# Kernel tuning notes

Hardware: AMD Instinct MI355X
Metric: run time of the kernel (lower is better)

## Reference

```python
import jax, jax.numpy as jnp
import numpy as np

N, M, D = 8192, 8192, 512

def setup_inputs() -> dict:
    key = jax.random.key(0)
    kx, ky = jax.random.split(key)
    x = jax.random.normal(kx, (N, D), dtype=jnp.float32)
    y = jax.random.normal(ky, (M, D), dtype=jnp.float32)
    gamma = jnp.ones((1,), dtype=jnp.float32)
    return {"x": x, "y": y, "gamma": gamma}

def reference(x, y, gamma):
    # Flatten leading dims as in the torch module
    x = x.reshape(-1, x.shape[-1])  # (N, D)
    y = y.reshape(-1, y.shape[-1])  # (M, D)
    x2 = jnp.sum(x * x, axis=-1)  # (N,)
    y2 = jnp.sum(y * y, axis=-1)  # (M,)
    xy = jnp.einsum('nd,md->nm', x, y)  # (N, M)
    sq_norm = x2[:, None] + y2[None, :] - 2.0 * xy
    return jnp.exp(-gamma[0] * sq_norm)
```

## Files before the change

kernel.cpp:

```cpp
#include <hip/hip_runtime.h>

#define NROWS 8192
#define DDIM  512
#define OUTN  8192

typedef int   i32x4  __attribute__((ext_vector_type(4)));
typedef int   i32x8  __attribute__((ext_vector_type(8)));
typedef float f32x16 __attribute__((ext_vector_type(16)));

__global__ void __launch_bounds__(256)
rbf_prep(const float* __restrict__ x, const float* __restrict__ y,
         unsigned char* __restrict__ xs, unsigned char* __restrict__ ys,
         float* __restrict__ x2, float* __restrict__ y2) {
    __shared__ unsigned char lbuf[16384];
    const int tid  = threadIdx.x;
    const int lane = tid & 63;
    const int w    = tid >> 6;

    int grp = blockIdx.x;
    const float* src; unsigned char* dst; float* nrm;
    if (grp < 256) { src = x; dst = xs; nrm = x2; }
    else           { grp -= 256; src = y; dst = ys; nrm = y2; }

    const int loff_base = (lane >> 3) * 2048 + ((lane >> 2) & 1) * 1024 + (lane & 3) * 8;

#pragma unroll
    for (int j = 0; j < 8; ++j) {
        const int r   = w * 8 + j;
        const int row = grp * 32 + r;
        const float* p = src + (size_t)row * DDIM + lane * 8;
        float4 v0 = *(const float4*)(p);
        float4 v1 = *(const float4*)(p + 4);

        float s = v0.x * v0.x + v0.y * v0.y + v0.z * v0.z + v0.w * v0.w
                + v1.x * v1.x + v1.y * v1.y + v1.z * v1.z + v1.w * v1.w;

        int lo = __builtin_amdgcn_cvt_pk_fp8_f32(v0.x, v0.y, 0, false);
        lo     = __builtin_amdgcn_cvt_pk_fp8_f32(v0.z, v0.w, lo, true);
        int hi = __builtin_amdgcn_cvt_pk_fp8_f32(v1.x, v1.y, 0, false);
        hi     = __builtin_amdgcn_cvt_pk_fp8_f32(v1.z, v1.w, hi, true);

        *(int2*)(lbuf + loff_base + r * 32) = make_int2(lo, hi);

#pragma unroll
        for (int o = 32; o > 0; o >>= 1) s += __shfl_down(s, o, 64);
        if (lane == 0) nrm[row] = s;
    }

    __syncthreads();
    unsigned char* gdst = dst + (size_t)grp * 16384;
#pragma unroll
    for (int it = 0; it < 4; ++it)
        *(i32x4*)(gdst + it * 4096 + tid * 16) =
            *(const i32x4*)(lbuf + it * 4096 + tid * 16);
}

__global__ void __launch_bounds__(256, 3)
rbf_gemm(const unsigned char* __restrict__ xs,
         const unsigned char* __restrict__ ys,
         const float* __restrict__ x2, const float* __restrict__ y2,
         const float* __restrict__ gamma, float* __restrict__ out) {
    const int tid  = threadIdx.x;
    const int lane = tid & 63;
    const int w    = tid >> 6;
    const int wm   = w & 1;
    const int wn   = w >> 1;

    const int bm = blockIdx.x & 63;
    const int bn = blockIdx.x >> 6;
    const int row0 = bm * 128;
    const int col0 = bn * 128;

    f32x16 acc[2][2] = {};

    const unsigned char* abase = xs + (size_t)(bm * 4 + wm * 2) * 16384 + lane * 32;
    const unsigned char* bbase = ys + (size_t)(bn * 4 + wn * 2) * 16384 + lane * 32;

#pragma unroll 2
    for (int h = 0; h < 8; ++h) {
        i32x8 af[2], bf[2];
#pragma unroll
        for (int mi = 0; mi < 2; ++mi) {
            const unsigned char* p = abase + mi * 16384 + h * 2048;
            i32x4 lo = *(const i32x4*)(p);
            i32x4 hi = *(const i32x4*)(p + 16);
            af[mi] = __builtin_shufflevector(lo, hi, 0, 1, 2, 3, 4, 5, 6, 7);
        }
#pragma unroll
        for (int ni = 0; ni < 2; ++ni) {
            const unsigned char* p = bbase + ni * 16384 + h * 2048;
            i32x4 lo = *(const i32x4*)(p);
            i32x4 hi = *(const i32x4*)(p + 16);
            bf[ni] = __builtin_shufflevector(lo, hi, 0, 1, 2, 3, 4, 5, 6, 7);
        }
#pragma unroll
        for (int mi = 0; mi < 2; ++mi)
#pragma unroll
            for (int ni = 0; ni < 2; ++ni)
                acc[mi][ni] = __builtin_amdgcn_mfma_scale_f32_32x32x64_f8f6f4(
                    af[mi], bf[ni], acc[mi][ni],
                    0, 0,
                    0, 0x7F,
                    0, 0x7F);
    }

    const float g  = gamma[0];
    const int   rq = (lane >> 5) * 4;
    const int   cl = lane & 31;
#pragma unroll
    for (int mi = 0; mi < 2; ++mi) {
        const int rbase = row0 + wm * 64 + mi * 32;
        float xn[16];
#pragma unroll
        for (int r = 0; r < 16; ++r)
            xn[r] = x2[rbase + (r & 3) + 8 * (r >> 2) + rq];
#pragma unroll
        for (int ni = 0; ni < 2; ++ni) {
            const int col = col0 + wn * 64 + ni * 32 + cl;
            const float yn = y2[col];
#pragma unroll
            for (int r = 0; r < 16; ++r) {
                const int row = rbase + (r & 3) + 8 * (r >> 2) + rq;
                const float s = xn[r] + yn - 2.0f * acc[mi][ni][r];
                __builtin_nontemporal_store(__expf(-g * s),
                                            out + (size_t)row * OUTN + col);
            }
        }
    }
}

extern "C" void kernel_launch(void* const* d_in, const int* in_sizes, int n_in,
                              void* d_out, int out_size, void* d_ws, size_t ws_size,
                              hipStream_t stream) {
    const float* x     = (const float*)d_in[0];
    const float* y     = (const float*)d_in[1];
    const float* gamma = (const float*)d_in[2];
    float* out = (float*)d_out;

    char* ws = (char*)d_ws;
    unsigned char* xs = (unsigned char*)ws;
    unsigned char* ys = (unsigned char*)(ws + (size_t)NROWS * DDIM);
    float* x2 = (float*)(ws + (size_t)NROWS * DDIM * 2);
    float* y2 = (float*)(ws + (size_t)NROWS * DDIM * 2 + NROWS * 4);

    rbf_prep<<<512, 256, 0, stream>>>(x, y, xs, ys, x2, y2);
    rbf_gemm<<<4096, 256, 0, stream>>>(xs, ys, x2, y2, gamma, out);
}
```

Measured before the change: 303.8 us.

## Fully unroll FP8 GEMM loop, raise occupancy bound, set MFMA priority, vectorize norm loads

Raises the occupancy hint of the fused GEMM kernel from 3 to 4 blocks per SIMD budget and fully unrolls the K loop using incrementing pointers. MFMA issue is wrapped in s_setprio to favour matrix instructions, and row norms are loaded as float4 instead of scalar loads. This aims to hide global-load latency with more waves and fewer address computations, at the risk of register spilling under the tighter register cap.

```diff
diff --git a/kernel.cpp b/kernel.cpp
--- a/kernel.cpp
+++ b/kernel.cpp
@@ -55,7 +55,7 @@
             *(const i32x4*)(lbuf + it * 4096 + tid * 16);
 }
 
-__global__ void __launch_bounds__(256, 3)
+__global__ void __launch_bounds__(256, 4)
 rbf_gemm(const unsigned char* __restrict__ xs,
          const unsigned char* __restrict__ ys,
          const float* __restrict__ x2, const float* __restrict__ y2,
@@ -73,35 +73,38 @@
 
     f32x16 acc[2][2] = {};
 
-    const unsigned char* abase = xs + (size_t)(bm * 4 + wm * 2) * 16384 + lane * 32;
-    const unsigned char* bbase = ys + (size_t)(bn * 4 + wn * 2) * 16384 + lane * 32;
+    const unsigned char* pa0 = xs + (size_t)(bm * 4 + wm * 2) * 16384 + lane * 32;
+    const unsigned char* pa1 = pa0 + 16384;
+    const unsigned char* pb0 = ys + (size_t)(bn * 4 + wn * 2) * 16384 + lane * 32;
+    const unsigned char* pb1 = pb0 + 16384;
 
-#pragma unroll 2
+#pragma unroll
     for (int h = 0; h < 8; ++h) {
-        i32x8 af[2], bf[2];
-#pragma unroll
-        for (int mi = 0; mi < 2; ++mi) {
-            const unsigned char* p = abase + mi * 16384 + h * 2048;
-            i32x4 lo = *(const i32x4*)(p);
-            i32x4 hi = *(const i32x4*)(p + 16);
-            af[mi] = __builtin_shufflevector(lo, hi, 0, 1, 2, 3, 4, 5, 6, 7);
-        }
-#pragma unroll
-        for (int ni = 0; ni < 2; ++ni) {
-            const unsigned char* p = bbase + ni * 16384 + h * 2048;
-            i32x4 lo = *(const i32x4*)(p);
-            i32x4 hi = *(const i32x4*)(p + 16);
-            bf[ni] = __builtin_shufflevector(lo, hi, 0, 1, 2, 3, 4, 5, 6, 7);
-        }
-#pragma unroll
-        for (int mi = 0; mi < 2; ++mi)
-#pragma unroll
-            for (int ni = 0; ni < 2; ++ni)
-                acc[mi][ni] = __builtin_amdgcn_mfma_scale_f32_32x32x64_f8f6f4(
-                    af[mi], bf[ni], acc[mi][ni],
-                    0, 0,
-                    0, 0x7F,
-                    0, 0x7F);
+        i32x4 a0l = *(const i32x4*)(pa0);
+        i32x4 a0h = *(const i32x4*)(pa0 + 16);
+        i32x4 a1l = *(const i32x4*)(pa1);
+        i32x4 a1h = *(const i32x4*)(pa1 + 16);
+        i32x4 b0l = *(const i32x4*)(pb0);
+        i32x4 b0h = *(const i32x4*)(pb0 + 16);
+        i32x4 b1l = *(const i32x4*)(pb1);
+        i32x4 b1h = *(const i32x4*)(pb1 + 16);
+        i32x8 a0 = __builtin_shufflevector(a0l, a0h, 0, 1, 2, 3, 4, 5, 6, 7);
+        i32x8 a1 = __builtin_shufflevector(a1l, a1h, 0, 1, 2, 3, 4, 5, 6, 7);
+        i32x8 b0 = __builtin_shufflevector(b0l, b0h, 0, 1, 2, 3, 4, 5, 6, 7);
+        i32x8 b1 = __builtin_shufflevector(b1l, b1h, 0, 1, 2, 3, 4, 5, 6, 7);
+
+        __builtin_amdgcn_s_setprio(1);
+        acc[0][0] = __builtin_amdgcn_mfma_scale_f32_32x32x64_f8f6f4(
+            a0, b0, acc[0][0], 0, 0, 0, 0x7F, 0, 0x7F);
+        acc[0][1] = __builtin_amdgcn_mfma_scale_f32_32x32x64_f8f6f4(
+            a0, b1, acc[0][1], 0, 0, 0, 0x7F, 0, 0x7F);
+        acc[1][0] = __builtin_amdgcn_mfma_scale_f32_32x32x64_f8f6f4(
+            a1, b0, acc[1][0], 0, 0, 0, 0x7F, 0, 0x7F);
+        acc[1][1] = __builtin_amdgcn_mfma_scale_f32_32x32x64_f8f6f4(
+            a1, b1, acc[1][1], 0, 0, 0, 0x7F, 0, 0x7F);
+        __builtin_amdgcn_s_setprio(0);
+
+        pa0 += 2048; pa1 += 2048; pb0 += 2048; pb1 += 2048;
     }
 
     const float g  = gamma[0];
@@ -110,10 +113,10 @@
 #pragma unroll
     for (int mi = 0; mi < 2; ++mi) {
         const int rbase = row0 + wm * 64 + mi * 32;
-        float xn[16];
+        float4 xn4[4];
 #pragma unroll
-        for (int r = 0; r < 16; ++r)
-            xn[r] = x2[rbase + (r & 3) + 8 * (r >> 2) + rq];
+        for (int q = 0; q < 4; ++q)
+            xn4[q] = *(const float4*)(x2 + rbase + rq + q * 8);
 #pragma unroll
         for (int ni = 0; ni < 2; ++ni) {
             const int col = col0 + wn * 64 + ni * 32 + cl;
@@ -121,7 +124,7 @@
 #pragma unroll
             for (int r = 0; r < 16; ++r) {
                 const int row = rbase + (r & 3) + 8 * (r >> 2) + rq;
-                const float s = xn[r] + yn - 2.0f * acc[mi][ni][r];
+                const float s = xn4[r >> 2][r & 3] + yn - 2.0f * acc[mi][ni][r];
                 __builtin_nontemporal_store(__expf(-g * s),
                                             out + (size_t)row * OUTN + col);
             }
```

Measured after the change: 304.4 us. About the same (+0.2%).
